# Kernel tuning notes

Hardware: AMD Instinct MI355X
Metric: run time of the kernel (lower is better)

The kernel has to match this reference:

```python
import jax, jax.numpy as jnp
import numpy as np

VOCAB = 50257
B, L = 16384, 512


def setup_inputs() -> dict:
    key = jax.random.key(0)
    k1, k2 = jax.random.split(key)
    batch = jax.random.randint(k1, (B, L), 0, VOCAB, dtype=jnp.int64 if jax.config.jax_enable_x64 else jnp.int32)
    r = jax.random.normal(k2, (VOCAB,), dtype=jnp.float32)
    return {"batch": batch, "r": r, "n_positive": 120000, "n_negative": 100000}


def reference(batch, r, n_positive, n_negative):
    # bag-of-words features: counts[i, v] = #{j : batch[i, j] == v}
    # counts @ r == sum over tokens of r[token]  (fused gather-and-sum,
    # mathematically identical to the dense scatter+matmul in the original)
    scores = jnp.sum(jnp.take(r, batch, axis=0), axis=-1)  # [B]
    log_prior = jnp.log(jnp.float32(n_positive) / jnp.float32(n_negative))
    return scores + log_prior
```

## Files before the change

kernel.cpp:

```cpp
#include <hip/hip_runtime.h>
#include <hip/hip_bf16.h>


#define B_ROWS 16384
#define L_TOK  512
#define WAVES_PER_BLOCK 4

typedef int v4i __attribute__((ext_vector_type(4)));

__global__ __launch_bounds__(256) void nb_score_kernel(
    const int* __restrict__ batch,
    const float* __restrict__ r,
    const int* __restrict__ n_pos,
    const int* __restrict__ n_neg,
    float* __restrict__ out)
{
    const int lane = threadIdx.x & 63;
    const int wave = threadIdx.x >> 6;
    const int row  = blockIdx.x * WAVES_PER_BLOCK + wave;
    if (row >= B_ROWS) return;

    const v4i* bp = reinterpret_cast<const v4i*>(batch + (size_t)row * L_TOK);

    v4i t0 = __builtin_nontemporal_load(&bp[lane]);
    v4i t1 = __builtin_nontemporal_load(&bp[64 + lane]);

    float g0 = r[t0.x];
    float g1 = r[t0.y];
    float g2 = r[t0.z];
    float g3 = r[t0.w];
    float g4 = r[t1.x];
    float g5 = r[t1.y];
    float g6 = r[t1.z];
    float g7 = r[t1.w];

    float acc = ((g0 + g1) + (g2 + g3)) + ((g4 + g5) + (g6 + g7));

#pragma unroll
    for (int off = 32; off > 0; off >>= 1)
        acc += __shfl_xor(acc, off, 64);

    if (lane == 0) {
        float log_prior = logf((float)n_pos[0] / (float)n_neg[0]);
        __builtin_nontemporal_store(acc + log_prior, &out[row]);
    }
}

extern "C" void kernel_launch(void* const* d_in, const int* in_sizes, int n_in,
                              void* d_out, int out_size, void* d_ws, size_t ws_size,
                              hipStream_t stream) {
    const int*   batch = (const int*)d_in[0];
    const float* r     = (const float*)d_in[1];
    const int*   n_pos = (const int*)d_in[2];
    const int*   n_neg = (const int*)d_in[3];
    float*       out   = (float*)d_out;

    dim3 grid(B_ROWS / WAVES_PER_BLOCK);
    dim3 block(64 * WAVES_PER_BLOCK);
    nb_score_kernel<<<grid, block, 0, stream>>>(batch, r, n_pos, n_neg, out);
}
```

Measured before the change: 109.1 us.

## Stage most of the score table in LDS and gather from shared memory

Adds a kernel that copies the first 40960 entries of r (160 KB) into dynamic LDS per 1024-thread block, then processes 64 rows per block. Token lookups below that cutoff read LDS, and the rest fall back to global memory. The aim is to move random gathers off the L2/global path. In exchange, every one of 256 blocks pays a 160 KB staging copy and a barrier, and occupancy is limited to one block per CU. The original kernel is kept as a fallback if the large-LDS attribute cannot be set.

```diff
diff --git a/kernel.cpp b/kernel.cpp
--- a/kernel.cpp
+++ b/kernel.cpp
@@ -2,17 +2,73 @@
 #include <hip/hip_bf16.h>
 
 
-#define B_ROWS 16384
-#define L_TOK  512
+#define B_ROWS   16384
+#define L_TOK    512
+#define VOCAB    50257
+#define C_ENTRIES 40960
+#define LDS_BYTES (C_ENTRIES * 4)
+
+typedef int   v4i __attribute__((ext_vector_type(4)));
+typedef float v4f __attribute__((ext_vector_type(4)));
+
+#define BLK_T   1024
+#define ROWS_PB 64
+#define GRID_B  (B_ROWS / ROWS_PB)
+
+static_assert(B_ROWS % ROWS_PB == 0, "grid divides rows");
+static_assert((C_ENTRIES / 4) % BLK_T == 0, "staging loop exact");
+static_assert(L_TOK == 64 * 4 * 2, "two v4i loads per lane per row");
+
+__global__ __launch_bounds__(BLK_T, 1) void nb_lds_kernel(
+    const int* __restrict__ batch, const float* __restrict__ r,
+    const int* __restrict__ n_pos, const int* __restrict__ n_neg,
+    float* __restrict__ out)
+{
+    extern __shared__ float rs[];
+
+    {
+        const v4f* r4 = reinterpret_cast<const v4f*>(r);
+        v4f* rs4 = reinterpret_cast<v4f*>(rs);
+#pragma unroll
+        for (int i = 0; i < C_ENTRIES / 4 / BLK_T; ++i)
+            rs4[i * BLK_T + threadIdx.x] = r4[i * BLK_T + threadIdx.x];
+    }
+    __syncthreads();
+
+    const int lane = threadIdx.x & 63;
+    const int wave = threadIdx.x >> 6;
+    const int row0 = blockIdx.x * ROWS_PB + wave * 4;
+
+    float log_prior = logf((float)n_pos[0] / (float)n_neg[0]);
+
+#pragma unroll
+    for (int k = 0; k < 4; ++k) {
+        const int row = row0 + k;
+        const v4i* bp = reinterpret_cast<const v4i*>(batch + (size_t)row * L_TOK);
+        v4i t0 = __builtin_nontemporal_load(&bp[lane]);
+        v4i t1 = __builtin_nontemporal_load(&bp[64 + lane]);
+
+        int idx[8] = { t0.x, t0.y, t0.z, t0.w, t1.x, t1.y, t1.z, t1.w };
+        float g[8];
+#pragma unroll
+        for (int e = 0; e < 8; ++e)
+            g[e] = (idx[e] < C_ENTRIES) ? rs[idx[e]] : r[idx[e]];
+
+        float acc = ((g[0] + g[1]) + (g[2] + g[3])) + ((g[4] + g[5]) + (g[6] + g[7]));
+#pragma unroll
+        for (int off = 32; off > 0; off >>= 1)
+            acc += __shfl_xor(acc, off, 64);
+
+        if (lane == 0)
+            __builtin_nontemporal_store(acc + log_prior, &out[row]);
+    }
+}
+
 #define WAVES_PER_BLOCK 4
 
-typedef int v4i __attribute__((ext_vector_type(4)));
-
 __global__ __launch_bounds__(256) void nb_score_kernel(
-    const int* __restrict__ batch,
-    const float* __restrict__ r,
-    const int* __restrict__ n_pos,
-    const int* __restrict__ n_neg,
+    const int* __restrict__ batch, const float* __restrict__ r,
+    const int* __restrict__ n_pos, const int* __restrict__ n_neg,
     float* __restrict__ out)
 {
     const int lane = threadIdx.x & 63;
@@ -21,21 +77,11 @@
     if (row >= B_ROWS) return;
 
     const v4i* bp = reinterpret_cast<const v4i*>(batch + (size_t)row * L_TOK);
-
     v4i t0 = __builtin_nontemporal_load(&bp[lane]);
     v4i t1 = __builtin_nontemporal_load(&bp[64 + lane]);
 
-    float g0 = r[t0.x];
-    float g1 = r[t0.y];
-    float g2 = r[t0.z];
-    float g3 = r[t0.w];
-    float g4 = r[t1.x];
-    float g5 = r[t1.y];
-    float g6 = r[t1.z];
-    float g7 = r[t1.w];
-
-    float acc = ((g0 + g1) + (g2 + g3)) + ((g4 + g5) + (g6 + g7));
-
+    float acc = ((r[t0.x] + r[t0.y]) + (r[t0.z] + r[t0.w]))
+              + ((r[t1.x] + r[t1.y]) + (r[t1.z] + r[t1.w]));
 #pragma unroll
     for (int off = 32; off > 0; off >>= 1)
         acc += __shfl_xor(acc, off, 64);
@@ -55,7 +101,14 @@
     const int*   n_neg = (const int*)d_in[3];
     float*       out   = (float*)d_out;
 
-    dim3 grid(B_ROWS / WAVES_PER_BLOCK);
-    dim3 block(64 * WAVES_PER_BLOCK);
-    nb_score_kernel<<<grid, block, 0, stream>>>(batch, r, n_pos, n_neg, out);
+    hipError_t e = hipFuncSetAttribute(
+        reinterpret_cast<const void*>(nb_lds_kernel),
+        hipFuncAttributeMaxDynamicSharedMemorySize, LDS_BYTES);
+
+    if (e == hipSuccess) {
+        nb_lds_kernel<<<GRID_B, BLK_T, LDS_BYTES, stream>>>(batch, r, n_pos, n_neg, out);
+    } else {
+        nb_score_kernel<<<B_ROWS / WAVES_PER_BLOCK, 64 * WAVES_PER_BLOCK, 0, stream>>>(
+            batch, r, n_pos, n_neg, out);
+    }
 }
```

Result: faster. 87.81 us (-19.5%).
